# Kernel optimization log

Hardware: AMD Instinct MI355X
Metric: run time of the kernel (lower is better)

## Reference

```python
import jax, jax.numpy as jnp
import numpy as np

VOCAB = 30522
EMBED = 768
NUM_CAT = 18
HIS = 50
CLICK_DIM = 100


def setup_inputs() -> dict:
    key = jax.random.key(0)
    ks = jax.random.split(key, 12)
    B, H, S = 64, HIS, 32
    encoding = jax.random.randint(ks[0], (B, H, S), 0, VOCAB)
    attention_mask = jnp.ones((B, H, S), dtype=bool)
    category_mask = jax.random.randint(ks[1], (B, NUM_CAT, H), 0, 2).astype(bool)
    inv = 1.0 / np.sqrt(EMBED)
    return {
        "encoding": encoding,
        "attention_mask": attention_mask,
        "category_mask": category_mask,
        "word_emb": jax.random.normal(ks[2], (VOCAB, EMBED), jnp.float32) * 0.02,
        "proj_w": jax.random.normal(ks[3], (EMBED, EMBED), jnp.float32) * inv,
        "proj_b": jnp.zeros((EMBED,), jnp.float32),
        "category_embedding": jax.random.normal(ks[4], (NUM_CAT, EMBED), jnp.float32) * 0.02,
        "w_news_attn": jax.random.normal(ks[5], (EMBED,), jnp.float32) * inv,
        "w_cat_attn": jax.random.normal(ks[6], (EMBED,), jnp.float32) * inv,
        "num_click_emb": jax.random.normal(ks[7], (HIS + 1, CLICK_DIM), jnp.float32) * 0.02,
        "click_w": jax.random.normal(ks[8], (CLICK_DIM,), jnp.float32) * (1.0 / np.sqrt(CLICK_DIM)),
        "click_b": jnp.zeros((), jnp.float32),
    }


def reference(encoding, attention_mask, category_mask, word_emb, proj_w, proj_b,
              category_embedding, w_news_attn, w_cat_attn, num_click_emb, click_w, click_b):
    # --- news_encoder stand-in: embedding lookup + masked mean pool + tanh(Linear) ---
    tok = word_emb[encoding]                                   # [B,H,S,E]
    m = attention_mask.astype(tok.dtype)[..., None]            # [B,H,S,1]
    pooled = (tok * m).sum(axis=2) / jnp.maximum(m.sum(axis=2), 1.0)  # [B,H,E]
    news_repr = jnp.tanh(pooled @ proj_w + proj_b)             # [B,H,E]

    # --- per-category masked softmax attention over history ---
    news_w = news_repr @ w_news_attn                           # [B,H]
    neg_inf = jnp.float32(-jnp.inf)
    scores = jnp.where(category_mask, news_w[:, None, :], neg_inf)  # [B,C,H]
    attn = jnp.nan_to_num(jax.nn.softmax(scores, axis=-1))     # nan rows (empty cats) -> 0
    category_interest = jnp.einsum('bch,bhe->bce', attn, news_repr)  # [B,C,E]
    category_repr = category_interest + category_embedding     # [B,C,E]

    # --- category-level attention with num-click scoring ---
    cat_w = category_repr @ w_cat_attn                          # [B,C]
    count = category_mask.sum(axis=-1).astype(jnp.int32)        # [B,C], <= HIS
    click_score = num_click_emb[count] @ click_w + click_b      # [B,C]
    final = cat_w + click_score
    final = jnp.where(count == 0, neg_inf, final)
    final = jax.nn.softmax(final, axis=-1)                      # [B,C]
    user_repr = jnp.einsum('bc,bce->be', final, category_repr)  # [B,E]
    return category_repr, user_repr
```

## Files before the change

### kernel.cpp

```cpp
#include <hip/hip_runtime.h>
#include <hip/hip_bf16.h>
#include <math.h>

#define VOCAB 30522
#define EMBED 768
#define NUM_CAT 18
#define HIS 50
#define SEQ 32
#define BATCH 64
#define CLICK_DIM 100

typedef short v8s __attribute__((ext_vector_type(8)));
typedef float v4f __attribute__((ext_vector_type(4)));
typedef unsigned short v8u __attribute__((ext_vector_type(8)));
typedef unsigned char v8c __attribute__((ext_vector_type(8)));

#define OFF_POOLED 0
#define OFF_WT     4915200
#define OFF_NR     6094848
#define OFF_NEWSW  15925248
#define OFF_FLAG   16177664
#define OFF_QTAB   16252928
#define OFF_DSCALE 39693824
#define WS_NEED    39815912ull

#define QBLKS 7631
#define TBLKS 576
#define PREP_GRID (QBLKS + TBLKS + 1)

__device__ __forceinline__ bool read_mask(const void* p, int i, int flag) {
    if (flag == 0) return ((const int*)p)[i] != 0;
    if (flag == 1) return ((const unsigned char*)p)[i] != 0;
    return ((const float*)p)[i] != 0.0f;
}

__device__ __forceinline__ float bf2f(unsigned short u) {
    union { unsigned int i; float f; } cv;
    cv.i = ((unsigned int)u) << 16;
    return cv.f;
}
__device__ __forceinline__ unsigned short f2bf(float f) {
    __hip_bfloat16 h = __float2bfloat16(f);
    return *(unsigned short*)&h;
}

__global__ __launch_bounds__(256) void kprep(
        const float* __restrict__ W, __hip_bfloat16* __restrict__ Wt,
        const unsigned int* __restrict__ cm, int* __restrict__ flag_out,
        const float* __restrict__ wemb, signed char* __restrict__ qtab,
        float* __restrict__ dscales, float* __restrict__ news_w) {
    int blk = blockIdx.x;
    if (blk < QBLKS) {
        int wv = threadIdx.x >> 6, lane = threadIdx.x & 63;
        int row = blk * 4 + wv;
        if (row < VOCAB) {
            const float4* src = (const float4*)(wemb + (size_t)row * EMBED);
            float4 v0 = src[lane], v1 = src[lane + 64], v2 = src[lane + 128];
            float mx = fmaxf(fmaxf(fabsf(v0.x), fabsf(v0.y)),
                             fmaxf(fabsf(v0.z), fabsf(v0.w)));
            mx = fmaxf(mx, fmaxf(fmaxf(fabsf(v1.x), fabsf(v1.y)),
                                 fmaxf(fabsf(v1.z), fabsf(v1.w))));
            mx = fmaxf(mx, fmaxf(fmaxf(fabsf(v2.x), fabsf(v2.y)),
                                 fmaxf(fabsf(v2.z), fabsf(v2.w))));
            #pragma unroll
            for (int off = 32; off; off >>= 1) mx = fmaxf(mx, __shfl_xor(mx, off));
            float inv = (mx > 0.f) ? 127.0f / mx : 0.f;
            signed char* qr = qtab + (size_t)row * EMBED;
            float4 vv[3] = {v0, v1, v2};
            #pragma unroll
            for (int i = 0; i < 3; ++i) {
                int q0 = max(-127, min(127, __float2int_rn(vv[i].x * inv)));
                int q1 = max(-127, min(127, __float2int_rn(vv[i].y * inv)));
                int q2 = max(-127, min(127, __float2int_rn(vv[i].z * inv)));
                int q3 = max(-127, min(127, __float2int_rn(vv[i].w * inv)));
                char4 c; c.x = (signed char)q0; c.y = (signed char)q1;
                c.z = (signed char)q2; c.w = (signed char)q3;
                *(char4*)(qr + i * 256 + lane * 4) = c;
            }
            if (lane == 0) dscales[row] = mx * (1.0f / 127.0f);
        }
    } else if (blk < QBLKS + TBLKS) {
        int tb = blk - QBLKS;
        __shared__ float t[32][33];
        int tx = threadIdx.x & 31, ty = threadIdx.x >> 5;
        int k0 = (tb % 24) * 32, n0 = (tb / 24) * 32;
        #pragma unroll
        for (int i = 0; i < 4; ++i)
            t[ty + i * 8][tx] = W[(size_t)(k0 + ty + i * 8) * EMBED + n0 + tx];
        __syncthreads();
        #pragma unroll
        for (int i = 0; i < 4; ++i)
            Wt[(size_t)(n0 + ty + i * 8) * EMBED + k0 + tx] =
                __float2bfloat16(t[tx][ty + i * 8]);
    } else {
        __shared__ int word_gt1, byte_gt1;
        if (threadIdx.x == 0) { word_gt1 = 0; byte_gt1 = 0; }
        __syncthreads();
        int lw = 0, lb = 0;
        for (int i = threadIdx.x; i < 14400; i += 256) {
            unsigned int v = cm[i];
            if (v > 1u) lw = 1;
            if ((v & 0xFFu) > 1u || ((v >> 8) & 0xFFu) > 1u ||
                ((v >> 16) & 0xFFu) > 1u || ((v >> 24) & 0xFFu) > 1u) lb = 1;
        }
        if (lw) atomicOr(&word_gt1, 1);
        if (lb) atomicOr(&byte_gt1, 1);
        for (int i = threadIdx.x; i < BATCH * HIS; i += 256) news_w[i] = 0.f;
        __syncthreads();
        if (threadIdx.x == 0) {
            int f = 0;
            if (word_gt1) f = byte_gt1 ? 2 : 1;
            *flag_out = f;
        }
    }
}

__global__ __launch_bounds__(192, 1) void k1c_pool(
        const int* __restrict__ enc, const void* amask,
        const unsigned char* __restrict__ qtab, const float* __restrict__ dscales,
        __hip_bfloat16* __restrict__ pooled, const int* __restrict__ flagp) {
    int tid = threadIdx.x, lane = tid & 63;
    int blk = blockIdx.x;
    int flag = *flagp;
    int bh0 = blk * 2, bh1 = blk * 2 + 1;
    bool mm = (lane < 32) ? read_mask(amask, bh0 * SEQ + lane, flag)
                          : read_mask(amask, bh1 * SEQ + (lane - 32), flag);
    unsigned long long bal = __ballot(mm);
    unsigned int mb0 = (unsigned int)(bal & 0xFFFFFFFFull);
    unsigned int mb1 = (unsigned int)(bal >> 32);
    int half = (tid >= 96) ? 1 : 0;
    int bh = half ? bh1 : bh0;
    unsigned int mb = half ? mb1 : mb0;
    float cnt = (float)__popc(mb);
    int slot = tid - half * 96;
    const int* e = enc + bh * SEQ;
    v8c v[SEQ];
    float ds[SEQ];
    #pragma unroll
    for (int j = 0; j < SEQ; ++j) {
        int tok = e[j];
        v[j] = ((const v8c*)(qtab + (size_t)tok * EMBED))[slot];
        ds[j] = dscales[tok];
    }
    float a[8] = {};
    #pragma unroll
    for (int j = 0; j < SEQ; ++j) {
        float msc = ((mb >> j) & 1u) ? ds[j] : 0.f;
        #pragma unroll
        for (int k = 0; k < 8; ++k) {
            int q = (int)(signed char)v[j][k];
            a[k] = fmaf((float)q, msc, a[k]);
        }
    }
    float d = 1.0f / fmaxf(cnt, 1.0f);
    v8u o;
    #pragma unroll
    for (int k = 0; k < 8; ++k) o[k] = f2bf(a[k] * d);
    *(v8u*)(((unsigned short*)pooled) + (size_t)bh * EMBED + slot * 8) = o;
}

__global__ __launch_bounds__(1024) void k0_detect(
        const unsigned int* __restrict__ cm, int* flag_out, float* __restrict__ news_w) {
    __shared__ int word_gt1, byte_gt1;
    if (threadIdx.x == 0) { word_gt1 = 0; byte_gt1 = 0; }
    __syncthreads();
    int lw = 0, lb = 0;
    for (int i = threadIdx.x; i < 14400; i += blockDim.x) {
        unsigned int v = cm[i];
        if (v > 1u) lw = 1;
        if ((v & 0xFFu) > 1u || ((v >> 8) & 0xFFu) > 1u ||
            ((v >> 16) & 0xFFu) > 1u || ((v >> 24) & 0xFFu) > 1u) lb = 1;
    }
    if (lw) atomicOr(&word_gt1, 1);
    if (lb) atomicOr(&byte_gt1, 1);
    for (int i = threadIdx.x; i < BATCH * HIS; i += blockDim.x) news_w[i] = 0.f;
    __syncthreads();
    if (threadIdx.x == 0) {
        int f = 0;
        if (word_gt1) f = byte_gt1 ? 2 : 1;
        *flag_out = f;
    }
}

__global__ __launch_bounds__(256) void k2a_wt(
        const float* __restrict__ W, __hip_bfloat16* __restrict__ Wt) {
    __shared__ float t[32][33];
    int tx = threadIdx.x & 31, ty = threadIdx.x >> 5;
    int k0 = blockIdx.x * 32, n0 = blockIdx.y * 32;
    #pragma unroll
    for (int i = 0; i < 4; ++i)
        t[ty + i * 8][tx] = W[(size_t)(k0 + ty + i * 8) * EMBED + n0 + tx];
    __syncthreads();
    #pragma unroll
    for (int i = 0; i < 4; ++i)
        Wt[(size_t)(n0 + ty + i * 8) * EMBED + k0 + tx] =
            __float2bfloat16(t[tx][ty + i * 8]);
}

__global__ __launch_bounds__(192) void k1_pool(
        const int* __restrict__ enc, const void* amask,
        const float* __restrict__ wemb, __hip_bfloat16* __restrict__ pooled,
        const int* __restrict__ flagp) {
    int wave = threadIdx.x >> 6, lane = threadIdx.x & 63;
    int bh = blockIdx.x;
    int flag = *flagp;
    const int* e = enc + bh * SEQ;
    bool m = (lane < SEQ) ? read_mask(amask, bh * SEQ + lane, flag) : false;
    unsigned long long mb = __ballot(m);
    float cnt = (float)__popcll(mb);
    int fslot = wave * 64 + lane;
    float ax = 0.f, ay = 0.f, az = 0.f, aw = 0.f;
    #pragma unroll
    for (int s0 = 0; s0 < SEQ; s0 += 8) {
        float4 v[8];
        #pragma unroll
        for (int j = 0; j < 8; ++j)
            v[j] = ((const float4*)(wemb + (size_t)e[s0 + j] * EMBED))[fslot];
        #pragma unroll
        for (int j = 0; j < 8; ++j) {
            float mmv = ((mb >> (s0 + j)) & 1ull) ? 1.0f : 0.0f;
            ax += mmv * v[j].x; ay += mmv * v[j].y;
            az += mmv * v[j].z; aw += mmv * v[j].w;
        }
    }
    float d = 1.0f / fmaxf(cnt, 1.0f);
    ushort4 pk;
    pk.x = f2bf(ax * d); pk.y = f2bf(ay * d);
    pk.z = f2bf(az * d); pk.w = f2bf(aw * d);
    *(ushort4*)((unsigned short*)pooled + (size_t)bh * EMBED + fslot * 4) = pk;
}

#define BM 64
#define BN 64
#define GBK 64
#define LDP 72
__global__ __launch_bounds__(256) void k2_mfma(
        const __hip_bfloat16* __restrict__ A,
        const __hip_bfloat16* __restrict__ Bt,
        const float* __restrict__ bias,
        const float* __restrict__ wna,
        unsigned short* __restrict__ C,
        float* __restrict__ news_w) {
    __shared__ short As[BM * LDP];
    __shared__ short Bs[BN * LDP];
    int tid = threadIdx.x;
    int wave = tid >> 6, lane = tid & 63;
    int l15 = lane & 15, l4 = lane >> 4;
    int wr = wave >> 1, wc = wave & 1;
    int row0 = blockIdx.x * BM;
    int col0 = blockIdx.y * BN;
    v4f acc[2][2] = {};

    int ra[2], ca[2];
    #pragma unroll
    for (int it = 0; it < 2; ++it) {
        int chunk = tid + it * 256;
        ra[it] = chunk >> 3; ca[it] = chunk & 7;
    }

    v8s pa[2], pb[2];
    #pragma unroll
    for (int it = 0; it < 2; ++it) {
        pa[it] = *(const v8s*)(A  + (size_t)(row0 + ra[it]) * EMBED + ca[it] * 8);
        pb[it] = *(const v8s*)(Bt + (size_t)(col0 + ra[it]) * EMBED + ca[it] * 8);
    }

    for (int s = 0; s < EMBED / GBK; ++s) {
        #pragma unroll
        for (int it = 0; it < 2; ++it) {
            *(v8s*)&As[ra[it] * LDP + ca[it] * 8] = pa[it];
            *(v8s*)&Bs[ra[it] * LDP + ca[it] * 8] = pb[it];
        }
        __syncthreads();
        if (s < EMBED / GBK - 1) {
            int k0 = (s + 1) * GBK;
            #pragma unroll
            for (int it = 0; it < 2; ++it) {
                pa[it] = *(const v8s*)(A  + (size_t)(row0 + ra[it]) * EMBED + k0 + ca[it] * 8);
                pb[it] = *(const v8s*)(Bt + (size_t)(col0 + ra[it]) * EMBED + k0 + ca[it] * 8);
            }
        }
        #pragma unroll
        for (int kk = 0; kk < 2; ++kk) {
            v8s af[2], bf_[2];
            #pragma unroll
            for (int mi = 0; mi < 2; ++mi)
                af[mi] = *(const v8s*)&As[(wr * 32 + mi * 16 + l15) * LDP + kk * 32 + l4 * 8];
            #pragma unroll
            for (int ni = 0; ni < 2; ++ni)
                bf_[ni] = *(const v8s*)&Bs[(wc * 32 + ni * 16 + l15) * LDP + kk * 32 + l4 * 8];
            #pragma unroll
            for (int mi = 0; mi < 2; ++mi)
                #pragma unroll
                for (int ni = 0; ni < 2; ++ni)
                    acc[mi][ni] = __builtin_amdgcn_mfma_f32_16x16x32_bf16(
                        af[mi], bf_[ni], acc[mi][ni], 0, 0, 0);
        }
        __syncthreads();
    }
    float bcol[2], wcol[2];
    #pragma unroll
    for (int ni = 0; ni < 2; ++ni) {
        int col = col0 + wc * 32 + ni * 16 + l15;
        bcol[ni] = bias[col]; wcol[ni] = wna[col];
    }
    #pragma unroll
    for (int mi = 0; mi < 2; ++mi) {
        #pragma unroll
        for (int r = 0; r < 4; ++r) {
            int row = row0 + wr * 32 + mi * 16 + l4 * 4 + r;
            float pr = 0.f;
            #pragma unroll
            for (int ni = 0; ni < 2; ++ni) {
                int col = col0 + wc * 32 + ni * 16 + l15;
                float tv = tanhf(acc[mi][ni][r] + bcol[ni]);
                C[(size_t)row * EMBED + col] = f2bf(tv);
                pr += tv * wcol[ni];
            }
            pr += __shfl_xor(pr, 1); pr += __shfl_xor(pr, 2);
            pr += __shfl_xor(pr, 4); pr += __shfl_xor(pr, 8);
            if (l15 == 0) atomicAdd(&news_w[row], pr);
        }
    }
}

__global__ __launch_bounds__(768) void k4_fused(
        const void* cmask, const unsigned short* __restrict__ nr,
        const float* __restrict__ news_w, const float* __restrict__ cat_emb,
        const float* __restrict__ w_cat, const float* __restrict__ click_emb,
        const float* __restrict__ click_w, const float* __restrict__ click_b,
        float* __restrict__ out_cat, float* __restrict__ user,
        const int* __restrict__ flagp) {
    int b = blockIdx.x, tid = threadIdx.x;
    int wave = tid >> 6, lane = tid & 63;
    int flag = *flagp;
    __shared__ float plds[HIS][20];
    __shared__ float redbuf[NUM_CAT][12];
    __shared__ float clicks[NUM_CAT];
    __shared__ int   cnts[NUM_CAT];
    __shared__ float logit[NUM_CAT];

    for (int c = wave; c < NUM_CAT; c += 12) {
        bool m = false; float v = -INFINITY;
        if (lane < HIS) {
            m = read_mask(cmask, (b * NUM_CAT + c) * HIS + lane, flag);
            if (m) v = news_w[b * HIS + lane];
        }
        unsigned long long bal = __ballot(m);
        int cnt = __popcll(bal);
        float maxv = v;
        #pragma unroll
        for (int off = 32; off; off >>= 1) maxv = fmaxf(maxv, __shfl_xor(maxv, off));
        float e = (v == -INFINITY) ? 0.f : expf(v - maxv);
        float sum = e;
        #pragma unroll
        for (int off = 32; off; off >>= 1) sum += __shfl_xor(sum, off);
        if (lane < HIS)
            plds[lane][c] = (cnt == 0 || v == -INFINITY) ? 0.f : e / sum;
        float cs = 0.f;
        if (lane < HIS) {
            const float* ce = click_emb + (size_t)cnt * CLICK_DIM;
            cs = ce[lane] * click_w[lane] + ce[lane + HIS] * click_w[lane + HIS];
        }
        #pragma unroll
        for (int off = 32; off; off >>= 1) cs += __shfl_down(cs, off);
        if (lane == 0) { cnts[c] = cnt; clicks[c] = cs + click_b[0]; }
    }
    __syncthreads();

    int col = tid;
    const unsigned short* nrb = nr + (size_t)b * HIS * EMBED;
    float acc[NUM_CAT];
    #pragma unroll
    for (int c = 0; c < NUM_CAT; ++c) acc[c] = 0.f;
    #pragma unroll 5
    for (int h = 0; h < HIS; ++h) {
        float v = bf2f(nrb[h * EMBED + col]);
        #pragma unroll
        for (int c = 0; c < NUM_CAT; ++c) acc[c] += plds[h][c] * v;
    }
    float part[NUM_CAT];
    float wv = w_cat[col];
    float* ocb = out_cat + (size_t)b * NUM_CAT * EMBED;
    #pragma unroll
    for (int c = 0; c < NUM_CAT; ++c) {
        float o = acc[c] + cat_emb[c * EMBED + col];
        acc[c] = o;
        ocb[c * EMBED + col] = o;
        part[c] = o * wv;
    }
    #pragma unroll
    for (int c = 0; c < NUM_CAT; ++c) {
        float s = part[c];
        #pragma unroll
        for (int off = 32; off; off >>= 1) s += __shfl_down(s, off);
        if (lane == 0) redbuf[c][wave] = s;
    }
    __syncthreads();
    if (tid < NUM_CAT) {
        float s = 0.f;
        #pragma unroll
        for (int w = 0; w < 12; ++w) s += redbuf[tid][w];
        logit[tid] = (cnts[tid] == 0) ? -INFINITY : (s + clicks[tid]);
    }
    __syncthreads();

    float maxv = -INFINITY;
    #pragma unroll
    for (int c = 0; c < NUM_CAT; ++c) maxv = fmaxf(maxv, logit[c]);
    float sum = 0.f;
    #pragma unroll
    for (int c = 0; c < NUM_CAT; ++c)
        sum += (logit[c] == -INFINITY) ? 0.f : expf(logit[c] - maxv);
    float u = 0.f;
    #pragma unroll
    for (int c = 0; c < NUM_CAT; ++c) {
        float w = (logit[c] == -INFINITY) ? 0.f : expf(logit[c] - maxv) / sum;
        u += w * acc[c];
    }
    user[(size_t)b * EMBED + col] = u;
}

extern "C" void kernel_launch(void* const* d_in, const int* in_sizes, int n_in,
                              void* d_out, int out_size, void* d_ws, size_t ws_size,
                              hipStream_t stream) {
    const int*   enc    = (const int*)d_in[0];
    const void*  amask  = d_in[1];
    const void*  cmask  = d_in[2];
    const float* wemb   = (const float*)d_in[3];
    const float* projw  = (const float*)d_in[4];
    const float* projb  = (const float*)d_in[5];
    const float* catemb = (const float*)d_in[6];
    const float* wna    = (const float*)d_in[7];
    const float* wca    = (const float*)d_in[8];
    const float* clemb  = (const float*)d_in[9];
    const float* clw    = (const float*)d_in[10];
    const float* clb    = (const float*)d_in[11];

    unsigned char* wsb = (unsigned char*)d_ws;
    __hip_bfloat16* pooled = (__hip_bfloat16*)(wsb + OFF_POOLED);
    __hip_bfloat16* Wt     = (__hip_bfloat16*)(wsb + OFF_WT);
    unsigned short* nr     = (unsigned short*)(wsb + OFF_NR);
    float* news_w = (float*)(wsb + OFF_NEWSW);
    int*   flag   = (int*)(wsb + OFF_FLAG);
    signed char* qtab = (signed char*)(wsb + OFF_QTAB);
    float* dscales = (float*)(wsb + OFF_DSCALE);

    float* out_cat = (float*)d_out;
    float* user    = (float*)d_out + BATCH * NUM_CAT * EMBED;

    if (ws_size >= WS_NEED) {
        kprep<<<PREP_GRID, 256, 0, stream>>>(
            projw, Wt, (const unsigned int*)cmask, flag, wemb, qtab, dscales, news_w);
        k1c_pool<<<1600, 192, 0, stream>>>(enc, amask, (const unsigned char*)qtab,
                                           dscales, pooled, flag);
    } else {
        k0_detect<<<1, 1024, 0, stream>>>((const unsigned int*)cmask, flag, news_w);
        dim3 gt(24, 24);
        k2a_wt<<<gt, 256, 0, stream>>>(projw, Wt);
        k1_pool<<<3200, 192, 0, stream>>>(enc, amask, wemb, pooled, flag);
    }
    dim3 g2(50, 12);
    k2_mfma<<<g2, 256, 0, stream>>>(pooled, Wt, projb, wna, nr, news_w);
    k4_fused<<<BATCH, 768, 0, stream>>>(cmask, nr, news_w, catemb, wca,
                                        clemb, clw, clb, out_cat, user, flag);
}
```

Measured before the change: 78.97 us.

## Fuse all stages into one cooperative persistent kernel with grid syncs

```diff
diff --git a/kernel.cpp b/kernel.cpp
--- a/kernel.cpp
+++ b/kernel.cpp
@@ -1,6 +1,9 @@
 #include <hip/hip_runtime.h>
 #include <hip/hip_bf16.h>
+#include <hip/hip_cooperative_groups.h>
 #include <math.h>
+
+namespace cg = cooperative_groups;
 
 #define VOCAB 30522
 #define EMBED 768
@@ -42,6 +45,335 @@
 __device__ __forceinline__ unsigned short f2bf(float f) {
     __hip_bfloat16 h = __float2bfloat16(f);
     return *(unsigned short*)&h;
+}
+
+#define BM 64
+#define BN 64
+#define GBK 64
+#define LDP 72
+
+__global__ __launch_bounds__(256, 2) void kmega(
+        const float* W, __hip_bfloat16* Wt, const unsigned int* cm, int* flag_out,
+        const float* wemb, signed char* qtab, float* dscales, float* news_w,
+        const int* enc, const void* amask, __hip_bfloat16* pooled,
+        const float* bias, const float* wna, unsigned short* nr,
+        const void* cmask, const float* cat_emb, const float* w_cat,
+        const float* click_emb, const float* click_w, const float* click_b,
+        float* out_cat, float* user) {
+    alignas(16) __shared__ char smem[18464];
+    cg::grid_group grid = cg::this_grid();
+    int tid = threadIdx.x;
+    int wave = tid >> 6, lane = tid & 63;
+    int gsz = gridDim.x;
+
+    for (int vb = blockIdx.x; vb < PREP_GRID; vb += gsz) {
+        if (vb < QBLKS) {
+            int row = vb * 4 + wave;
+            if (row < VOCAB) {
+                const float4* src = (const float4*)(wemb + (size_t)row * EMBED);
+                float4 v0 = src[lane], v1 = src[lane + 64], v2 = src[lane + 128];
+                float mx = fmaxf(fmaxf(fabsf(v0.x), fabsf(v0.y)),
+                                 fmaxf(fabsf(v0.z), fabsf(v0.w)));
+                mx = fmaxf(mx, fmaxf(fmaxf(fabsf(v1.x), fabsf(v1.y)),
+                                     fmaxf(fabsf(v1.z), fabsf(v1.w))));
+                mx = fmaxf(mx, fmaxf(fmaxf(fabsf(v2.x), fabsf(v2.y)),
+                                     fmaxf(fabsf(v2.z), fabsf(v2.w))));
+                #pragma unroll
+                for (int off = 32; off; off >>= 1) mx = fmaxf(mx, __shfl_xor(mx, off));
+                float inv = (mx > 0.f) ? 127.0f / mx : 0.f;
+                signed char* qr = qtab + (size_t)row * EMBED;
+                float4 vv[3] = {v0, v1, v2};
+                #pragma unroll
+                for (int i = 0; i < 3; ++i) {
+                    int q0 = max(-127, min(127, __float2int_rn(vv[i].x * inv)));
+                    int q1 = max(-127, min(127, __float2int_rn(vv[i].y * inv)));
+                    int q2 = max(-127, min(127, __float2int_rn(vv[i].z * inv)));
+                    int q3 = max(-127, min(127, __float2int_rn(vv[i].w * inv)));
+                    char4 c; c.x = (signed char)q0; c.y = (signed char)q1;
+                    c.z = (signed char)q2; c.w = (signed char)q3;
+                    *(char4*)(qr + i * 256 + lane * 4) = c;
+                }
+                if (lane == 0) dscales[row] = mx * (1.0f / 127.0f);
+            }
+        } else if (vb < QBLKS + TBLKS) {
+            float (*t)[33] = (float(*)[33])smem;
+            int tb = vb - QBLKS;
+            int tx = tid & 31, ty = tid >> 5;
+            int k0 = (tb % 24) * 32, n0 = (tb / 24) * 32;
+            #pragma unroll
+            for (int i = 0; i < 4; ++i)
+                t[ty + i * 8][tx] = W[(size_t)(k0 + ty + i * 8) * EMBED + n0 + tx];
+            __syncthreads();
+            #pragma unroll
+            for (int i = 0; i < 4; ++i)
+                Wt[(size_t)(n0 + ty + i * 8) * EMBED + k0 + tx] =
+                    __float2bfloat16(t[tx][ty + i * 8]);
+            __syncthreads();
+        } else {
+            int* wg = (int*)smem;
+            if (tid == 0) { wg[0] = 0; wg[1] = 0; }
+            __syncthreads();
+            int lw = 0, lb = 0;
+            for (int i = tid; i < 14400; i += 256) {
+                unsigned int v = cm[i];
+                if (v > 1u) lw = 1;
+                if ((v & 0xFFu) > 1u || ((v >> 8) & 0xFFu) > 1u ||
+                    ((v >> 16) & 0xFFu) > 1u || ((v >> 24) & 0xFFu) > 1u) lb = 1;
+            }
+            if (lw) atomicOr(&wg[0], 1);
+            if (lb) atomicOr(&wg[1], 1);
+            for (int i = tid; i < BATCH * HIS; i += 256) news_w[i] = 0.f;
+            __syncthreads();
+            if (tid == 0) {
+                int f = 0;
+                if (wg[0]) f = wg[1] ? 2 : 1;
+                *flag_out = f;
+            }
+            __syncthreads();
+        }
+    }
+    __threadfence();
+    grid.sync();
+
+    int flag = *flag_out;
+
+    for (int vb = blockIdx.x; vb < 800; vb += gsz) {
+        int bh = vb * 4 + wave;
+        bool m = (lane < SEQ) ? read_mask(amask, bh * SEQ + lane, flag) : false;
+        unsigned int mb = (unsigned int)(__ballot(m) & 0xFFFFFFFFull);
+        float cnt = (float)__popc(mb);
+        const int* e = enc + bh * SEQ;
+        char4 v[4][3]; float ds4[4];
+        #pragma unroll
+        for (int j = 0; j < 4; ++j) {
+            int tok = e[j];
+            const char4* qr = (const char4*)(qtab + (size_t)tok * EMBED);
+            #pragma unroll
+            for (int k = 0; k < 3; ++k) v[j][k] = qr[lane + 64 * k];
+            ds4[j] = dscales[tok];
+        }
+        float a[12] = {};
+        #pragma unroll
+        for (int s0 = 0; s0 < SEQ; s0 += 4) {
+            char4 w[4][3]; float dw[4];
+            if (s0 + 4 < SEQ) {
+                #pragma unroll
+                for (int j = 0; j < 4; ++j) {
+                    int tok = e[s0 + 4 + j];
+                    const char4* qr = (const char4*)(qtab + (size_t)tok * EMBED);
+                    #pragma unroll
+                    for (int k = 0; k < 3; ++k) w[j][k] = qr[lane + 64 * k];
+                    dw[j] = dscales[tok];
+                }
+            }
+            #pragma unroll
+            for (int j = 0; j < 4; ++j) {
+                float sc = ((mb >> (s0 + j)) & 1u) ? ds4[j] : 0.f;
+                #pragma unroll
+                for (int k = 0; k < 3; ++k) {
+                    a[k * 4 + 0] = fmaf((float)v[j][k].x, sc, a[k * 4 + 0]);
+                    a[k * 4 + 1] = fmaf((float)v[j][k].y, sc, a[k * 4 + 1]);
+                    a[k * 4 + 2] = fmaf((float)v[j][k].z, sc, a[k * 4 + 2]);
+                    a[k * 4 + 3] = fmaf((float)v[j][k].w, sc, a[k * 4 + 3]);
+                }
+            }
+            #pragma unroll
+            for (int j = 0; j < 4; ++j) {
+                #pragma unroll
+                for (int k = 0; k < 3; ++k) v[j][k] = w[j][k];
+                ds4[j] = dw[j];
+            }
+        }
+        float d = 1.0f / fmaxf(cnt, 1.0f);
+        unsigned short* prow = (unsigned short*)pooled + (size_t)bh * EMBED;
+        #pragma unroll
+        for (int k = 0; k < 3; ++k) {
+            ushort4 pk;
+            pk.x = f2bf(a[k * 4 + 0] * d); pk.y = f2bf(a[k * 4 + 1] * d);
+            pk.z = f2bf(a[k * 4 + 2] * d); pk.w = f2bf(a[k * 4 + 3] * d);
+            *(ushort4*)(prow + (size_t)(lane + 64 * k) * 4) = pk;
+        }
+    }
+    __threadfence();
+    grid.sync();
+
+    {
+        short* As = (short*)smem;
+        short* Bs = (short*)(smem + 9216);
+        int l15 = lane & 15, l4 = lane >> 4;
+        int wr = wave >> 1, wc = wave & 1;
+        const __hip_bfloat16* A = pooled;
+        const __hip_bfloat16* Bt = (const __hip_bfloat16*)Wt;
+        for (int vb = blockIdx.x; vb < 600; vb += gsz) {
+            int row0 = (vb % 50) * BM;
+            int col0 = (vb / 50) * BN;
+            v4f acc[2][2] = {};
+            int ra[2], ca[2];
+            #pragma unroll
+            for (int it = 0; it < 2; ++it) {
+                int chunk = tid + it * 256;
+                ra[it] = chunk >> 3; ca[it] = chunk & 7;
+            }
+            v8s pa[2], pb[2];
+            #pragma unroll
+            for (int it = 0; it < 2; ++it) {
+                pa[it] = *(const v8s*)(A  + (size_t)(row0 + ra[it]) * EMBED + ca[it] * 8);
+                pb[it] = *(const v8s*)(Bt + (size_t)(col0 + ra[it]) * EMBED + ca[it] * 8);
+            }
+            for (int s = 0; s < EMBED / GBK; ++s) {
+                #pragma unroll
+                for (int it = 0; it < 2; ++it) {
+                    *(v8s*)&As[ra[it] * LDP + ca[it] * 8] = pa[it];
+                    *(v8s*)&Bs[ra[it] * LDP + ca[it] * 8] = pb[it];
+                }
+                __syncthreads();
+                if (s < EMBED / GBK - 1) {
+                    int k0 = (s + 1) * GBK;
+                    #pragma unroll
+                    for (int it = 0; it < 2; ++it) {
+                        pa[it] = *(const v8s*)(A  + (size_t)(row0 + ra[it]) * EMBED + k0 + ca[it] * 8);
+                        pb[it] = *(const v8s*)(Bt + (size_t)(col0 + ra[it]) * EMBED + k0 + ca[it] * 8);
+                    }
+                }
+                #pragma unroll
+                for (int kk = 0; kk < 2; ++kk) {
+                    v8s af[2], bf_[2];
+                    #pragma unroll
+                    for (int mi = 0; mi < 2; ++mi)
+                        af[mi] = *(const v8s*)&As[(wr * 32 + mi * 16 + l15) * LDP + kk * 32 + l4 * 8];
+                    #pragma unroll
+                    for (int ni = 0; ni < 2; ++ni)
+                        bf_[ni] = *(const v8s*)&Bs[(wc * 32 + ni * 16 + l15) * LDP + kk * 32 + l4 * 8];
+                    #pragma unroll
+                    for (int mi = 0; mi < 2; ++mi)
+                        #pragma unroll
+                        for (int ni = 0; ni < 2; ++ni)
+                            acc[mi][ni] = __builtin_amdgcn_mfma_f32_16x16x32_bf16(
+                                af[mi], bf_[ni], acc[mi][ni], 0, 0, 0);
+                }
+                __syncthreads();
+            }
+            float bcol[2], wcol[2];
+            #pragma unroll
+            for (int ni = 0; ni < 2; ++ni) {
+                int col = col0 + wc * 32 + ni * 16 + l15;
+                bcol[ni] = bias[col]; wcol[ni] = wna[col];
+            }
+            #pragma unroll
+            for (int mi = 0; mi < 2; ++mi) {
+                #pragma unroll
+                for (int r = 0; r < 4; ++r) {
+                    int row = row0 + wr * 32 + mi * 16 + l4 * 4 + r;
+                    float pr = 0.f;
+                    #pragma unroll
+                    for (int ni = 0; ni < 2; ++ni) {
+                        int col = col0 + wc * 32 + ni * 16 + l15;
+                        float tv = tanhf(acc[mi][ni][r] + bcol[ni]);
+                        nr[(size_t)row * EMBED + col] = f2bf(tv);
+                        pr += tv * wcol[ni];
+                    }
+                    pr += __shfl_xor(pr, 1); pr += __shfl_xor(pr, 2);
+                    pr += __shfl_xor(pr, 4); pr += __shfl_xor(pr, 8);
+                    if (l15 == 0) atomicAdd(&news_w[row], pr);
+                }
+            }
+        }
+    }
+    __threadfence();
+    grid.sync();
+
+    {
+        float* plds   = (float*)smem;
+        float* redbuf = (float*)(smem + 4000);
+        float* clicks = (float*)(smem + 4288);
+        int*   cnts   = (int*)(smem + 4360);
+        float* logit  = (float*)(smem + 4432);
+        for (int vb = blockIdx.x; vb < BATCH; vb += gsz) {
+            int b = vb;
+            for (int c = wave; c < NUM_CAT; c += 4) {
+                bool m = false; float v = -INFINITY;
+                if (lane < HIS) {
+                    m = read_mask(cmask, (b * NUM_CAT + c) * HIS + lane, flag);
+                    if (m) v = news_w[b * HIS + lane];
+                }
+                unsigned long long bal = __ballot(m);
+                int cnt = __popcll(bal);
+                float maxv = v;
+                #pragma unroll
+                for (int off = 32; off; off >>= 1) maxv = fmaxf(maxv, __shfl_xor(maxv, off));
+                float e = (v == -INFINITY) ? 0.f : expf(v - maxv);
+                float sum = e;
+                #pragma unroll
+                for (int off = 32; off; off >>= 1) sum += __shfl_xor(sum, off);
+                if (lane < HIS)
+                    plds[lane * 20 + c] = (cnt == 0 || v == -INFINITY) ? 0.f : e / sum;
+                float cs = 0.f;
+                if (lane < HIS) {
+                    const float* ce = click_emb + (size_t)cnt * CLICK_DIM;
+                    cs = ce[lane] * click_w[lane] + ce[lane + HIS] * click_w[lane + HIS];
+                }
+                #pragma unroll
+                for (int off = 32; off; off >>= 1) cs += __shfl_down(cs, off);
+                if (lane == 0) { cnts[c] = cnt; clicks[c] = cs + click_b[0]; }
+            }
+            __syncthreads();
+
+            const unsigned short* nrb = nr + (size_t)b * HIS * EMBED;
+            float acc0[NUM_CAT] = {}, acc1[NUM_CAT] = {}, acc2[NUM_CAT] = {};
+            #pragma unroll 2
+            for (int h = 0; h < HIS; ++h) {
+                float v0 = bf2f(nrb[h * EMBED + tid]);
+                float v1 = bf2f(nrb[h * EMBED + tid + 256]);
+                float v2 = bf2f(nrb[h * EMBED + tid + 512]);
+                #pragma unroll
+                for (int c = 0; c < NUM_CAT; ++c) {
+                    float p = plds[h * 20 + c];
+                    acc0[c] = fmaf(p, v0, acc0[c]);
+                    acc1[c] = fmaf(p, v1, acc1[c]);
+                    acc2[c] = fmaf(p, v2, acc2[c]);
+                }
+            }
+            float wv0 = w_cat[tid], wv1 = w_cat[tid + 256], wv2 = w_cat[tid + 512];
+            float* ocb = out_cat + (size_t)b * NUM_CAT * EMBED;
+            #pragma unroll
+            for (int c = 0; c < NUM_CAT; ++c) {
+                float o0 = acc0[c] + cat_emb[c * EMBED + tid];
+                float o1 = acc1[c] + cat_emb[c * EMBED + tid + 256];
+                float o2 = acc2[c] + cat_emb[c * EMBED + tid + 512];
+                acc0[c] = o0; acc1[c] = o1; acc2[c] = o2;
+                ocb[c * EMBED + tid]       = o0;
+                ocb[c * EMBED + tid + 256] = o1;
+                ocb[c * EMBED + tid + 512] = o2;
+                float s = o0 * wv0 + o1 * wv1 + o2 * wv2;
+                #pragma unroll
+                for (int off = 32; off; off >>= 1) s += __shfl_down(s, off);
+                if (lane == 0) redbuf[c * 4 + wave] = s;
+            }
+            __syncthreads();
+            if (tid < NUM_CAT) {
+                float s = redbuf[tid * 4] + redbuf[tid * 4 + 1]
+                        + redbuf[tid * 4 + 2] + redbuf[tid * 4 + 3];
+                logit[tid] = (cnts[tid] == 0) ? -INFINITY : (s + clicks[tid]);
+            }
+            __syncthreads();
+            float maxv = -INFINITY;
+            #pragma unroll
+            for (int c = 0; c < NUM_CAT; ++c) maxv = fmaxf(maxv, logit[c]);
+            float sum = 0.f;
+            #pragma unroll
+            for (int c = 0; c < NUM_CAT; ++c)
+                sum += (logit[c] == -INFINITY) ? 0.f : expf(logit[c] - maxv);
+            float u0 = 0.f, u1 = 0.f, u2 = 0.f;
+            #pragma unroll
+            for (int c = 0; c < NUM_CAT; ++c) {
+                float w = (logit[c] == -INFINITY) ? 0.f : expf(logit[c] - maxv) / sum;
+                u0 += w * acc0[c]; u1 += w * acc1[c]; u2 += w * acc2[c];
+            }
+            float* ub = user + (size_t)b * EMBED;
+            ub[tid] = u0; ub[tid + 256] = u1; ub[tid + 512] = u2;
+            __syncthreads();
+        }
+    }
 }
 
 __global__ __launch_bounds__(256) void kprep(
@@ -115,7 +447,7 @@
     }
 }
 
-__global__ __launch_bounds__(192, 1) void k1c_pool(
+__global__ __launch_bounds__(192) void k1c_pool(
         const int* __restrict__ enc, const void* amask,
         const unsigned char* __restrict__ qtab, const float* __restrict__ dscales,
         __hip_bfloat16* __restrict__ pooled, const int* __restrict__ flagp) {
@@ -134,23 +466,36 @@
     float cnt = (float)__popc(mb);
     int slot = tid - half * 96;
     const int* e = enc + bh * SEQ;
-    v8c v[SEQ];
-    float ds[SEQ];
-    #pragma unroll
-    for (int j = 0; j < SEQ; ++j) {
+    float a[8] = {};
+    v8c v[8], w[8];
+    float ds[8], dw[8];
+    #pragma unroll
+    for (int j = 0; j < 8; ++j) {
         int tok = e[j];
         v[j] = ((const v8c*)(qtab + (size_t)tok * EMBED))[slot];
         ds[j] = dscales[tok];
     }
-    float a[8] = {};
-    #pragma unroll
-    for (int j = 0; j < SEQ; ++j) {
-        float msc = ((mb >> j) & 1u) ? ds[j] : 0.f;
-        #pragma unroll
-        for (int k = 0; k < 8; ++k) {
-            int q = (int)(signed char)v[j][k];
-            a[k] = fmaf((float)q, msc, a[k]);
-        }
+    #pragma unroll
+    for (int s0 = 0; s0 < SEQ; s0 += 8) {
+        if (s0 + 8 < SEQ) {
+            #pragma unroll
+            for (int j = 0; j < 8; ++j) {
+                int tok = e[s0 + 8 + j];
+                w[j] = ((const v8c*)(qtab + (size_t)tok * EMBED))[slot];
+                dw[j] = dscales[tok];
+            }
+        }
+        #pragma unroll
+        for (int j = 0; j < 8; ++j) {
+            float msc = ((mb >> (s0 + j)) & 1u) ? ds[j] : 0.f;
+            #pragma unroll
+            for (int k = 0; k < 8; ++k) {
+                int q = (int)(signed char)v[j][k];
+                a[k] = fmaf((float)q, msc, a[k]);
+            }
+        }
+        #pragma unroll
+        for (int j = 0; j < 8; ++j) { v[j] = w[j]; ds[j] = dw[j]; }
     }
     float d = 1.0f / fmaxf(cnt, 1.0f);
     v8u o;
@@ -230,10 +575,6 @@
     *(ushort4*)((unsigned short*)pooled + (size_t)bh * EMBED + fslot * 4) = pk;
 }
 
-#define BM 64
-#define BN 64
-#define GBK 64
-#define LDP 72
 __global__ __launch_bounds__(256) void k2_mfma(
         const __hip_bfloat16* __restrict__ A,
         const __hip_bfloat16* __restrict__ Bt,
@@ -250,21 +591,18 @@
     int row0 = blockIdx.x * BM;
     int col0 = blockIdx.y * BN;
     v4f acc[2][2] = {};
-
     int ra[2], ca[2];
     #pragma unroll
     for (int it = 0; it < 2; ++it) {
         int chunk = tid + it * 256;
         ra[it] = chunk >> 3; ca[it] = chunk & 7;
     }
-
     v8s pa[2], pb[2];
     #pragma unroll
     for (int it = 0; it < 2; ++it) {
         pa[it] = *(const v8s*)(A  + (size_t)(row0 + ra[it]) * EMBED + ca[it] * 8);
         pb[it] = *(const v8s*)(Bt + (size_t)(col0 + ra[it]) * EMBED + ca[it] * 8);
     }
-
     for (int s = 0; s < EMBED / GBK; ++s) {
         #pragma unroll
         for (int it = 0; it < 2; ++it) {
@@ -339,7 +677,6 @@
     __shared__ float clicks[NUM_CAT];
     __shared__ int   cnts[NUM_CAT];
     __shared__ float logit[NUM_CAT];
-
     for (int c = wave; c < NUM_CAT; c += 12) {
         bool m = false; float v = -INFINITY;
         if (lane < HIS) {
@@ -367,7 +704,6 @@
         if (lane == 0) { cnts[c] = cnt; clicks[c] = cs + click_b[0]; }
     }
     __syncthreads();
-
     int col = tid;
     const unsigned short* nrb = nr + (size_t)b * HIS * EMBED;
     float acc[NUM_CAT];
@@ -404,7 +740,6 @@
         logit[tid] = (cnts[tid] == 0) ? -INFINITY : (s + clicks[tid]);
     }
     __syncthreads();
-
     float maxv = -INFINITY;
     #pragma unroll
     for (int c = 0; c < NUM_CAT; ++c) maxv = fmaxf(maxv, logit[c]);
@@ -436,6 +771,7 @@
     const float* clemb  = (const float*)d_in[9];
     const float* clw    = (const float*)d_in[10];
     const float* clb    = (const float*)d_in[11];
+    const unsigned int* cmu = (const unsigned int*)cmask;
 
     unsigned char* wsb = (unsigned char*)d_ws;
     __hip_bfloat16* pooled = (__hip_bfloat16*)(wsb + OFF_POOLED);
@@ -450,18 +786,42 @@
     float* user    = (float*)d_out + BATCH * NUM_CAT * EMBED;
 
     if (ws_size >= WS_NEED) {
-        kprep<<<PREP_GRID, 256, 0, stream>>>(
-            projw, Wt, (const unsigned int*)cmask, flag, wemb, qtab, dscales, news_w);
-        k1c_pool<<<1600, 192, 0, stream>>>(enc, amask, (const unsigned char*)qtab,
-                                           dscales, pooled, flag);
+        int maxb = 0;
+        hipError_t oe = hipOccupancyMaxActiveBlocksPerMultiprocessor(
+            &maxb, (const void*)kmega, 256, 0);
+        int grid = 512;
+        if (oe == hipSuccess && maxb >= 1) {
+            grid = maxb * 256;
+            if (grid > 600) grid = 600;
+        }
+        void* args[] = {
+            (void*)&projw, (void*)&Wt, (void*)&cmu, (void*)&flag,
+            (void*)&wemb, (void*)&qtab, (void*)&dscales, (void*)&news_w,
+            (void*)&enc, (void*)&amask, (void*)&pooled,
+            (void*)&projb, (void*)&wna, (void*)&nr,
+            (void*)&cmask, (void*)&catemb, (void*)&wca,
+            (void*)&clemb, (void*)&clw, (void*)&clb,
+            (void*)&out_cat, (void*)&user };
+        hipError_t err = hipLaunchCooperativeKernel(
+            (void*)kmega, dim3(grid), dim3(256), args, 0, stream);
+        if (err != hipSuccess) {
+            kprep<<<PREP_GRID, 256, 0, stream>>>(
+                projw, Wt, cmu, flag, wemb, qtab, dscales, news_w);
+            k1c_pool<<<1600, 192, 0, stream>>>(enc, amask, (const unsigned char*)qtab,
+                                               dscales, pooled, flag);
+            dim3 g2(50, 12);
+            k2_mfma<<<g2, 256, 0, stream>>>(pooled, Wt, projb, wna, nr, news_w);
+            k4_fused<<<BATCH, 768, 0, stream>>>(cmask, nr, news_w, catemb, wca,
+                                                clemb, clw, clb, out_cat, user, flag);
+        }
     } else {
-        k0_detect<<<1, 1024, 0, stream>>>((const unsigned int*)cmask, flag, news_w);
+        k0_detect<<<1, 1024, 0, stream>>>(cmu, flag, news_w);
         dim3 gt(24, 24);
         k2a_wt<<<gt, 256, 0, stream>>>(projw, Wt);
         k1_pool<<<3200, 192, 0, stream>>>(enc, amask, wemb, pooled, flag);
-    }
-    dim3 g2(50, 12);
-    k2_mfma<<<g2, 256, 0, stream>>>(pooled, Wt, projb, wna, nr, news_w);
-    k4_fused<<<BATCH, 768, 0, stream>>>(cmask, nr, news_w, catemb, wca,
-                                        clemb, clw, clb, out_cat, user, flag);
-}
+        dim3 g2(50, 12);
+        k2_mfma<<<g2, 256, 0, stream>>>(pooled, Wt, projb, wna, nr, news_w);
+        k4_fused<<<BATCH, 768, 0, stream>>>(cmask, nr, news_w, catemb, wca,
+                                            clemb, clw, clb, out_cat, user, flag);
+    }
+}
```

New measurement: 285.0 us. 261% more time.
